# Kernel tuning notes

Measured on AMD Instinct MI355X. Metric: run time of the kernel, lower is better.

Reference implementation:

```python
import jax, jax.numpy as jnp
import numpy as np

B = 4
HIDDEN = 256
NH, NL, NP = 8, 4, 4
DH = HIDDEN // NH
IMG = 256
SHAPES = ((64, 64), (32, 32), (16, 16), (8, 8))
CHS = (128, 256, 512, 512)
T = 3
NLAYERS = 6
S = sum(h * w for h, w in SHAPES)


def conv2d(x, w, b, pad):
    y = jax.lax.conv_general_dilated(x, w, (1, 1), [(pad, pad), (pad, pad)],
                                     dimension_numbers=('NCHW', 'OIHW', 'NCHW'))
    return y + b[None, :, None, None]


def group_norm(x, g, beta, groups=32, eps=1e-5):
    b, c, h, w = x.shape
    xg = x.reshape(b, groups, c // groups, h, w)
    mu = xg.mean((2, 3, 4), keepdims=True)
    var = ((xg - mu) ** 2).mean((2, 3, 4), keepdims=True)
    xg = (xg - mu) * jax.lax.rsqrt(var + eps)
    return xg.reshape(b, c, h, w) * g[None, :, None, None] + beta[None, :, None, None]


def layer_norm(x, g, b, eps=1e-5):
    mu = x.mean(-1, keepdims=True)
    var = ((x - mu) ** 2).mean(-1, keepdims=True)
    return (x - mu) * jax.lax.rsqrt(var + eps) * g + b


def pos_embed_sine(h, w, num_feats=128, temp=10000.0):
    # PositionEmbeddingSine with normalize=True, mask all-False
    scale = 2.0 * np.pi
    eps = 1e-6
    y = jnp.arange(1, h + 1, dtype=jnp.float32) / (h + eps) * scale
    x = jnp.arange(1, w + 1, dtype=jnp.float32) / (w + eps) * scale
    yy = jnp.broadcast_to(y[:, None], (h, w))
    xx = jnp.broadcast_to(x[None, :], (h, w))
    dim_t = temp ** (2.0 * (jnp.arange(num_feats) // 2).astype(jnp.float32) / num_feats)
    px = xx[..., None] / dim_t
    py = yy[..., None] / dim_t
    px = jnp.stack([jnp.sin(px[..., 0::2]), jnp.cos(px[..., 1::2])], -1).reshape(h, w, num_feats)
    py = jnp.stack([jnp.sin(py[..., 0::2]), jnp.cos(py[..., 1::2])], -1).reshape(h, w, num_feats)
    return jnp.concatenate([py, px], -1)  # (h, w, 2*num_feats)


def ms_deform(value, locs, attw):
    # value: (B,S,NH,DH); locs: (B,S,NH,NL,NP,2) normalized xy; attw: (B,S,NH,NL,NP)
    out = jnp.zeros((B, S, NH, DH), value.dtype)
    start = 0
    for l, (h, w) in enumerate(SHAPES):
        v = value[:, start:start + h * w]  # (B,hw,NH,DH)
        start += h * w
        gx = locs[:, :, :, l, :, 0] * w - 0.5  # grid_sample align_corners=False
        gy = locs[:, :, :, l, :, 1] * h - 0.5  # (B,S,NH,NP)
        x0 = jnp.floor(gx)
        y0 = jnp.floor(gy)
        wx1 = gx - x0
        wy1 = gy - y0
        acc = jnp.zeros((B, S, NH, NP, DH), value.dtype)
        for dy in (0, 1):
            for dx in (0, 1):
                xi = x0 + dx
                yi = y0 + dy
                wgt = (wx1 if dx else 1.0 - wx1) * (wy1 if dy else 1.0 - wy1)
                valid = ((xi >= 0) & (xi < w) & (yi >= 0) & (yi < h)).astype(value.dtype)
                xi_c = jnp.clip(xi, 0, w - 1).astype(jnp.int32)
                yi_c = jnp.clip(yi, 0, h - 1).astype(jnp.int32)
                idx = yi_c * w + xi_c  # (B,S,NH,NP)
                idx2 = idx.transpose(0, 1, 3, 2).reshape(B, S * NP, NH, 1)
                samp = jnp.take_along_axis(v, idx2, axis=1)  # (B,S*NP,NH,DH)
                samp = samp.reshape(B, S, NP, NH, DH).transpose(0, 1, 3, 2, 4)
                acc = acc + samp * (wgt * valid)[..., None]
        out = out + (acc * attw[:, :, :, l, :, None]).sum(3)
    return out.reshape(B, S, NH * DH)


def _forward(feat_t0_l0, feat_t0_l1, feat_t0_l2, feat_t0_l3,
             feat_t1_l0, feat_t1_l1, feat_t1_l2, feat_t1_l3,
             feat_t2_l0, feat_t2_l1, feat_t2_l2, feat_t2_l3,
             tfw,
             proj_w0, proj_b0, gn_g0, gn_b0,
             proj_w1, proj_b1, gn_g1, gn_b1,
             proj_w2, proj_b2, gn_g2, gn_b2,
             proj_w3, proj_b3, gn_g3, gn_b3,
             level_embed,
             off_w, off_b, aw_w, aw_b, val_w, val_b, out_w, out_b,
             ln1_g, ln1_b, ff1_w, ff1_b, ff2_w, ff2_b, ln2_g, ln2_b,
             c1_w, c1_b, c2_w, c2_b):
    feats = [[feat_t0_l0, feat_t0_l1, feat_t0_l2, feat_t0_l3],
             [feat_t1_l0, feat_t1_l1, feat_t1_l2, feat_t1_l3],
             [feat_t2_l0, feat_t2_l1, feat_t2_l2, feat_t2_l3]]
    proj = [(proj_w0, proj_b0, gn_g0, gn_b0), (proj_w1, proj_b1, gn_g1, gn_b1),
            (proj_w2, proj_b2, gn_g2, gn_b2), (proj_w3, proj_b3, gn_g3, gn_b3)]
    priors = (0, CHS[0], CHS[1], CHS[2])  # replicates original (buggy) prior indexing
    srcs, poss = [], []
    for l in range(NL):
        atf = jnp.stack([feats[t][l] for t in range(T)], 1)  # (B,T,C,H,W)
        wsl = jax.nn.softmax(tfw[:, priors[l]:priors[l] + CHS[l]], axis=0)  # (T,C)
        fused = (atf * wsl[None, :, :, None, None]).sum(1)
        pw, pb, gg, gb = proj[l]
        x = group_norm(conv2d(fused, pw, pb, 0), gg, gb)  # 1x1 proj + GN
        h, w = SHAPES[l]
        srcs.append(x.reshape(B, HIDDEN, h * w).transpose(0, 2, 1))
        pe = pos_embed_sine(h, w).reshape(h * w, HIDDEN) + level_embed[l]
        poss.append(jnp.broadcast_to(pe[None], (B, h * w, HIDDEN)))
    src = jnp.concatenate(srcs, 1)  # (B,S,256)
    pos = jnp.concatenate(poss, 1)
    # reference points (valid_ratios == 1 since masks are all False)
    refs = []
    for (h, w) in SHAPES:
        gy, gx = jnp.meshgrid((jnp.arange(h) + 0.5) / h, (jnp.arange(w) + 0.5) / w, indexing='ij')
        refs.append(jnp.stack([gx.ravel(), gy.ravel()], -1))
    ref = jnp.broadcast_to(jnp.concatenate(refs, 0)[None, :, None, :], (B, S, NL, 2)).astype(jnp.float32)
    norm_wh = jnp.array([[w, h] for (h, w) in SHAPES], jnp.float32)  # (NL,2) xy
    for i in range(NLAYERS):
        q = src + pos
        off = (q @ off_w[i].T + off_b[i]).reshape(B, S, NH, NL, NP, 2)
        aw = jax.nn.softmax((q @ aw_w[i].T + aw_b[i]).reshape(B, S, NH, NL * NP), -1).reshape(B, S, NH, NL, NP)
        val = (src @ val_w[i].T + val_b[i]).reshape(B, S, NH, DH)
        locs = ref[:, :, None, :, None, :] + off / norm_wh[None, None, None, :, None, :]
        attn = ms_deform(val, locs, aw) @ out_w[i].T + out_b[i]
        src = layer_norm(src + attn, ln1_g[i], ln1_b[i])
        ff = (jax.nn.relu(src @ ff1_w[i].T + ff1_b[i])) @ ff2_w[i].T + ff2_b[i]
        src = layer_norm(src + ff, ln2_g[i], ln2_b[i])
    h0, w0 = SHAPES[0]
    layer0 = src[:, :h0 * w0, :].reshape(B, h0, w0, HIDDEN).transpose(0, 3, 1, 2)
    pred = conv2d(jax.nn.relu(conv2d(layer0, c1_w, c1_b, 1)), c2_w, c2_b, 1)
    return jax.image.resize(pred, (B, pred.shape[1], IMG, IMG), method='bilinear')


def setup_inputs():
    key = jax.random.key(0)
    ks = iter(jax.random.split(key, 128))
    d = {}
    for t in range(T):
        for l, ((h, w), c) in enumerate(zip(SHAPES, CHS)):
            d['feat_t%d_l%d' % (t, l)] = jax.random.normal(next(ks), (B, c, h, w), jnp.float32)
    d['tfw'] = jax.random.normal(next(ks), (T, sum(CHS)), jnp.float32)
    for l, c in enumerate(CHS):
        d['proj_w%d' % l] = jax.random.normal(next(ks), (HIDDEN, c, 1, 1), jnp.float32) * 0.02
        d['proj_b%d' % l] = jnp.zeros((HIDDEN,), jnp.float32)
        d['gn_g%d' % l] = jnp.ones((HIDDEN,), jnp.float32)
        d['gn_b%d' % l] = jnp.zeros((HIDDEN,), jnp.float32)
    d['level_embed'] = jax.random.normal(next(ks), (NL, HIDDEN), jnp.float32)
    Lc = NLAYERS

    def w(shape, s=0.02):
        return jax.random.normal(next(ks), shape, jnp.float32) * s
    d['off_w'] = w((Lc, NH * NL * NP * 2, HIDDEN))
    d['off_b'] = w((Lc, NH * NL * NP * 2), 0.1)
    d['aw_w'] = w((Lc, NH * NL * NP, HIDDEN))
    d['aw_b'] = w((Lc, NH * NL * NP), 0.1)
    d['val_w'] = w((Lc, HIDDEN, HIDDEN))
    d['val_b'] = jnp.zeros((Lc, HIDDEN), jnp.float32)
    d['out_w'] = w((Lc, HIDDEN, HIDDEN))
    d['out_b'] = jnp.zeros((Lc, HIDDEN), jnp.float32)
    d['ln1_g'] = jnp.ones((Lc, HIDDEN), jnp.float32)
    d['ln1_b'] = jnp.zeros((Lc, HIDDEN), jnp.float32)
    d['ff1_w'] = w((Lc, 1024, HIDDEN))
    d['ff1_b'] = jnp.zeros((Lc, 1024), jnp.float32)
    d['ff2_w'] = w((Lc, HIDDEN, 1024))
    d['ff2_b'] = jnp.zeros((Lc, HIDDEN), jnp.float32)
    d['ln2_g'] = jnp.ones((Lc, HIDDEN), jnp.float32)
    d['ln2_b'] = jnp.zeros((Lc, HIDDEN), jnp.float32)
    d['c1_w'] = w((64, HIDDEN, 3, 3))
    d['c1_b'] = jnp.zeros((64,), jnp.float32)
    d['c2_w'] = w((2, 64, 3, 3))
    d['c2_b'] = jnp.zeros((2,), jnp.float32)
    return d


def reference(feat_t0_l0, feat_t0_l1, feat_t0_l2, feat_t0_l3,
              feat_t1_l0, feat_t1_l1, feat_t1_l2, feat_t1_l3,
              feat_t2_l0, feat_t2_l1, feat_t2_l2, feat_t2_l3,
              tfw,
              proj_w0, proj_b0, gn_g0, gn_b0,
              proj_w1, proj_b1, gn_g1, gn_b1,
              proj_w2, proj_b2, gn_g2, gn_b2,
              proj_w3, proj_b3, gn_g3, gn_b3,
              level_embed,
              off_w, off_b, aw_w, aw_b, val_w, val_b, out_w, out_b,
              ln1_g, ln1_b, ff1_w, ff1_b, ff2_w, ff2_b, ln2_g, ln2_b,
              c1_w, c1_b, c2_w, c2_b):
    return _forward(feat_t0_l0, feat_t0_l1, feat_t0_l2, feat_t0_l3,
                    feat_t1_l0, feat_t1_l1, feat_t1_l2, feat_t1_l3,
                    feat_t2_l0, feat_t2_l1, feat_t2_l2, feat_t2_l3,
                    tfw,
                    proj_w0, proj_b0, gn_g0, gn_b0,
                    proj_w1, proj_b1, gn_g1, gn_b1,
                    proj_w2, proj_b2, gn_g2, gn_b2,
                    proj_w3, proj_b3, gn_g3, gn_b3,
                    level_embed,
                    off_w, off_b, aw_w, aw_b, val_w, val_b, out_w, out_b,
                    ln1_g, ln1_b, ff1_w, ff1_b, ff2_w, ff2_b, ln2_g, ln2_b,
                    c1_w, c1_b, c2_w, c2_b)
```

## Files before the change

### kernel.cpp

```cpp
#include <hip/hip_runtime.h>
#include <math.h>

constexpr int kB = 4;
constexpr int kS = 5440;
constexpr int kH = 256;
constexpr int kNH = 8, kNL = 4, kNP = 4, kDH = 32;
constexpr int kM = kB * kS;
constexpr int kCHSUM = 1408;

typedef __attribute__((ext_vector_type(8))) short short8v;
typedef __attribute__((ext_vector_type(4))) short short4v;
typedef __attribute__((ext_vector_type(4))) float f32x4;

__device__ inline short bf16rne(float f) {
    unsigned u = __float_as_uint(f);
    u += 0x7FFF + ((u >> 16) & 1);
    return (short)(u >> 16);
}
__device__ inline float bf2f(short s) {
    return __uint_as_float(((unsigned)(unsigned short)s) << 16);
}


__global__ void f2bf_kernel(const float* __restrict__ in, short* __restrict__ out, int n)
{
    int idx = (blockIdx.x * blockDim.x + threadIdx.x) * 4;
    if (idx >= n) return;
    f32x4 v = *(const f32x4*)(in + idx);
    short4v o;
    o[0]=bf16rne(v[0]); o[1]=bf16rne(v[1]); o[2]=bf16rne(v[2]); o[3]=bf16rne(v[3]);
    *(short4v*)(out + idx) = o;
}

__global__ void concat_w_kernel(const float* __restrict__ off_w, const float* __restrict__ aw_w,
                                short* __restrict__ Wcat, int n)
{
    int idx = blockIdx.x * blockDim.x + threadIdx.x;
    if (idx >= n) return;
    int col = idx & 255;
    int row = (idx >> 8) % 384;
    int i   = idx / (384*256);
    float v = (row < 256) ? off_w[((size_t)i*256 + row)*256 + col]
                          : aw_w[((size_t)i*128 + row-256)*256 + col];
    Wcat[idx] = bf16rne(v);
}
__global__ void concat_b_kernel(const float* __restrict__ off_b, const float* __restrict__ aw_b,
                                float* __restrict__ bcat, int n)
{
    int idx = blockIdx.x * blockDim.x + threadIdx.x;
    if (idx >= n) return;
    int row = idx % 384;
    int i   = idx / 384;
    bcat[idx] = (row < 256) ? off_b[i*256 + row] : aw_b[i*128 + row-256];
}

__global__ void reorder_c1w_kernel(const float* __restrict__ w, short* __restrict__ out, int n)
{
    int idx = blockIdx.x * blockDim.x + threadIdx.x;
    if (idx >= n) return;
    int k = idx % 2304, o = idx / 2304;
    int kblk = k >> 8, c = k & 255;
    out[idx] = bf16rne(w[(size_t)o*2304 + c*9 + kblk]);
}
__global__ void reorder_c2w_kernel(const float* __restrict__ w, float* __restrict__ out)
{
    int idx = blockIdx.x * blockDim.x + threadIdx.x;
    if (idx >= 1152) return;
    int c = idx & 63, r = idx >> 6;
    int o = r / 9, kblk = r % 9;
    out[idx] = w[((size_t)o*64 + c)*9 + kblk];
}


__global__ __launch_bounds__(256) void fuseT_kernel(const float* __restrict__ f0,
        const float* __restrict__ f1, const float* __restrict__ f2,
        const float* __restrict__ tfw, short* __restrict__ out,
        int c, int hw, int prior)
{
    __shared__ float tile[32][33];
    int p0 = blockIdx.x * 32;
    int c0 = blockIdx.y * 32;
    int b  = blockIdx.z;
    int tx  = threadIdx.x & 31;
    int ty8 = threadIdx.x >> 5;
    #pragma unroll
    for (int i = 0; i < 4; ++i) {
        int ch = c0 + ty8 + i*8;
        float t0 = tfw[0*kCHSUM + prior + ch];
        float t1 = tfw[1*kCHSUM + prior + ch];
        float t2 = tfw[2*kCHSUM + prior + ch];
        float m = fmaxf(t0, fmaxf(t1, t2));
        float e0 = expf(t0-m), e1 = expf(t1-m), e2 = expf(t2-m);
        float inv = 1.0f / (e0+e1+e2);
        size_t base = ((size_t)b*c + ch)*hw + p0 + tx;
        tile[ty8+i*8][tx] = f0[base]*(e0*inv) + f1[base]*(e1*inv) + f2[base]*(e2*inv);
    }
    __syncthreads();
    #pragma unroll
    for (int i = 0; i < 4; ++i) {
        int p = p0 + ty8 + i*8;
        out[((size_t)b*hw + p)*c + c0 + tx] = bf16rne(tile[tx][ty8+i*8]);
    }
}

__global__ __launch_bounds__(256) void gn_sum_kernel(const float* __restrict__ xbufT,
        float* __restrict__ gnstat, int nchunks)
{
    int chunk = blockIdx.x, b = blockIdx.y;
    int t = threadIdx.x;
    size_t base = ((size_t)b*nchunks + chunk) * 4096;
    float s = 0.f, q = 0.f;
    #pragma unroll
    for (int i = 0; i < 4; ++i) {
        f32x4 v = *(const f32x4*)(xbufT + base + i*1024 + t*4);
        s += v[0]+v[1]+v[2]+v[3];
        q += v[0]*v[0]+v[1]*v[1]+v[2]*v[2]+v[3]*v[3];
    }
    __shared__ float ls[256], lq[256];
    ls[t] = s; lq[t] = q; __syncthreads();
    if (t < 64) { ls[t] += ls[t+64]+ls[t+128]+ls[t+192];
                  lq[t] += lq[t+64]+lq[t+128]+lq[t+192]; }
    __syncthreads();
    if (t < 32) {
        float ss = ls[2*t] + ls[2*t+1];
        float qq = lq[2*t] + lq[2*t+1];
        size_t o = (((size_t)b*nchunks + chunk)*32 + t)*2;
        gnstat[o] = ss; gnstat[o+1] = qq;
    }
}

__global__ __launch_bounds__(256) void gn_fin_kernel(const float* __restrict__ gnstat,
        const float* __restrict__ gg, const float* __restrict__ gb,
        float* __restrict__ gnA, float* __restrict__ gnB, int nchunks, int hw)
{
    int b = blockIdx.x, t = threadIdx.x;
    int g = t >> 3, sub = t & 7;
    float s = 0.f, q = 0.f;
    for (int c = sub; c < nchunks; c += 8) {
        size_t o = (((size_t)b*nchunks + c)*32 + g)*2;
        s += gnstat[o]; q += gnstat[o+1];
    }
    __shared__ float ls[256], lq[256], gmu[32], ginv[32];
    ls[t] = s; lq[t] = q; __syncthreads();
    if (sub < 4) { ls[t] += ls[t+4]; lq[t] += lq[t+4]; } __syncthreads();
    if (sub < 2) { ls[t] += ls[t+2]; lq[t] += lq[t+2]; } __syncthreads();
    if (sub == 0) {
        float ss = ls[t] + ls[t+1], qq = lq[t] + lq[t+1];
        float n = 8.0f * hw;
        float mu = ss / n;
        float var = qq / n - mu*mu;
        gmu[g] = mu; ginv[g] = rsqrtf(var + 1e-5f);
    }
    __syncthreads();
    int ch = t;
    float A = ginv[ch>>3] * gg[ch];
    float B = gb[ch] - gmu[ch>>3] * A;
    gnA[b*256 + ch] = A;
    gnB[b*256 + ch] = B;
}

__global__ __launch_bounds__(256) void gn_apply_kernel(const float* __restrict__ xbufT,
        const float* __restrict__ gnA, const float* __restrict__ gnB,
        const float* __restrict__ pos, float* __restrict__ src,
        short* __restrict__ srcbf, short* __restrict__ qbf, int hw, int sbase)
{
    int E = hw * 256;
    size_t fl = (size_t)blockIdx.x*1024 + threadIdx.x*4;
    int b = (int)(fl / E);
    int off = (int)(fl - (size_t)b*E);
    int p = off >> 8, col = off & 255;
    f32x4 v = *(const f32x4*)(xbufT + fl);
    f32x4 A = *(const f32x4*)(gnA + b*256 + col);
    f32x4 Bv = *(const f32x4*)(gnB + b*256 + col);
    size_t si = ((size_t)b*kS + sbase + p)*256 + col;
    f32x4 pv = *(const f32x4*)(pos + si);
    f32x4 o;
    o[0]=v[0]*A[0]+Bv[0]; o[1]=v[1]*A[1]+Bv[1];
    o[2]=v[2]*A[2]+Bv[2]; o[3]=v[3]*A[3]+Bv[3];
    *(f32x4*)(src + si) = o;
    short4v sb, qb;
    sb[0]=bf16rne(o[0]); sb[1]=bf16rne(o[1]); sb[2]=bf16rne(o[2]); sb[3]=bf16rne(o[3]);
    qb[0]=bf16rne(o[0]+pv[0]); qb[1]=bf16rne(o[1]+pv[1]);
    qb[2]=bf16rne(o[2]+pv[2]); qb[3]=bf16rne(o[3]+pv[3]);
    *(short4v*)(srcbf + si) = sb;
    *(short4v*)(qbf + si) = qb;
}

__global__ void pos_kernel(const float* __restrict__ lev, float* __restrict__ pos,
                           int h, int w, int sbase, int lvl, int n)
{
    int idx = blockIdx.x * blockDim.x + threadIdx.x;
    if (idx >= n) return;
    int ch = idx % kH;
    int p  = idx / kH;
    int py = p / w, px = p % w;
    int c2 = ch & 127;
    int i  = c2 >> 1;
    float invdt = exp2f((float)i * -0.20762050593046015f);
    float t;
    if (ch < 128) t = (py + 1) / ((float)h + 1e-6f) * 6.2831853071795864f;
    else          t = (px + 1) / ((float)w + 1e-6f) * 6.2831853071795864f;
    float arg = t * invdt;
    float val = (c2 & 1) ? cosf(arg) : sinf(arg);
    val += lev[lvl*kH + ch];
    for (int b = 0; b < kB; ++b)
        pos[((size_t)b*kS + sbase + p)*kH + ch] = val;
}

template<int BN, int OUTMODE>
__global__ __launch_bounds__(256) void gemm_big(const short* __restrict__ A,
        const short* __restrict__ W, const float* __restrict__ bias,
        float* __restrict__ C, short* __restrict__ Cb, int N, int K, int relu)
{
    constexpr int FJ = BN / 32;
    constexpr int NBV = (BN == 128) ? 4 : 2;
    __shared__ short Asm[2][128 * 40];
    __shared__ short Bsm[2][BN * 40];
    const int t    = threadIdx.x;
    const int bn   = blockIdx.x * BN;
    const int bm   = blockIdx.y * 128;
    const int lane = t & 63;
    const int wid  = t >> 6;
    const int wr   = wid >> 1;
    const int wc   = wid & 1;
    const int frow = lane & 15;
    const int g    = lane >> 4;
    const int sa_r = t >> 1;
    const int sa_p = t & 1;

    f32x4 acc[4][FJ];
    #pragma unroll
    for (int i = 0; i < 4; ++i)
        #pragma unroll
        for (int j = 0; j < FJ; ++j)
            acc[i][j] = (f32x4){0.f,0.f,0.f,0.f};

    const short* Aptr = A + (size_t)(bm + sa_r)*K + sa_p*32;
    short8v a[4], b[NBV];
    #pragma unroll
    for (int v = 0; v < 4; ++v) a[v] = *(const short8v*)(Aptr + v*8);

    int sb_r, sb_p, sb_o;
    const short* Wptr;
    if constexpr (BN == 128) {
        sb_r = t >> 1; sb_p = t & 1; sb_o = 0;
        Wptr = W + (size_t)(bn + sb_r)*K + sb_p*32;
    } else {
        sb_r = t >> 2; sb_p = (t & 3) >> 1; sb_o = (t & 1) * 16;
        Wptr = W + (size_t)(bn + sb_r)*K + (t & 3)*16;
    }
    #pragma unroll
    for (int v = 0; v < NBV; ++v) b[v] = *(const short8v*)(Wptr + v*8);

    for (int k0 = 0; k0 < K; k0 += 64) {
        __syncthreads();
        #pragma unroll
        for (int v = 0; v < 4; ++v) *(short8v*)&Asm[sa_p][sa_r*40 + v*8] = a[v];
        #pragma unroll
        for (int v = 0; v < NBV; ++v) *(short8v*)&Bsm[sb_p][sb_r*40 + sb_o + v*8] = b[v];
        __syncthreads();
        if (k0 + 64 < K) {
            #pragma unroll
            for (int v = 0; v < 4; ++v) a[v] = *(const short8v*)(Aptr + k0 + 64 + v*8);
            #pragma unroll
            for (int v = 0; v < NBV; ++v) b[v] = *(const short8v*)(Wptr + k0 + 64 + v*8);
        }
        #pragma unroll
        for (int p = 0; p < 2; ++p) {
            short8v af[4], bfv[FJ];
            #pragma unroll
            for (int i = 0; i < 4; ++i)
                af[i] = *(const short8v*)&Asm[p][(wr*64 + i*16 + frow)*40 + g*8];
            #pragma unroll
            for (int j = 0; j < FJ; ++j)
                bfv[j] = *(const short8v*)&Bsm[p][(wc*(BN/2) + j*16 + frow)*40 + g*8];
            #pragma unroll
            for (int i = 0; i < 4; ++i)
                #pragma unroll
                for (int j = 0; j < FJ; ++j)
                    acc[i][j] = __builtin_amdgcn_mfma_f32_16x16x32_bf16(af[i], bfv[j], acc[i][j], 0, 0, 0);
        }
    }

    #pragma unroll
    for (int j = 0; j < FJ; ++j) {
        int col = bn + wc*(BN/2) + j*16 + frow;
        float bz = bias[col];
        #pragma unroll
        for (int i = 0; i < 4; ++i) {
            int row = bm + wr*64 + i*16 + g*4;
            #pragma unroll
            for (int rr = 0; rr < 4; ++rr) {
                float v = acc[i][j][rr] + bz;
                if (relu) v = fmaxf(v, 0.f);
                if constexpr (OUTMODE == 0) C[(size_t)(row + rr)*N + col] = v;
                else                        Cb[(size_t)(row + rr)*N + col] = bf16rne(v);
            }
        }
    }
}

__global__ __launch_bounds__(256) void gemm_qv(const short* __restrict__ Aq,
        const short* __restrict__ As, const short* __restrict__ W1,
        const short* __restrict__ W2, const float* __restrict__ b1,
        const float* __restrict__ b2, float* __restrict__ C1,
        short* __restrict__ Cb2)
{
    __shared__ short Asm[2][128 * 40];
    __shared__ short Bsm[2][128 * 40];
    const int t    = threadIdx.x;
    const int bn   = blockIdx.x * 128;
    const int bm   = blockIdx.y * 128;
    const bool qreg = bn < 384;
    const int K = 256;
    const int lane = t & 63;
    const int wid  = t >> 6;
    const int wr   = wid >> 1;
    const int wc   = wid & 1;
    const int frow = lane & 15;
    const int g    = lane >> 4;
    const int sa_r = t >> 1;
    const int sa_p = t & 1;

    f32x4 acc[4][4];
    #pragma unroll
    for (int i = 0; i < 4; ++i)
        #pragma unroll
        for (int j = 0; j < 4; ++j)
            acc[i][j] = (f32x4){0.f,0.f,0.f,0.f};

    const short* Aptr = (qreg ? Aq : As) + (size_t)(bm + sa_r)*K + sa_p*32;
    const short* Wptr = (qreg ? (W1 + (size_t)(bn + sa_r)*K)
                              : (W2 + (size_t)(bn - 384 + sa_r)*K)) + sa_p*32;
    short8v a[4], b[4];
    #pragma unroll
    for (int v = 0; v < 4; ++v) { a[v] = *(const short8v*)(Aptr + v*8);
                                  b[v] = *(const short8v*)(Wptr + v*8); }

    for (int k0 = 0; k0 < K; k0 += 64) {
        __syncthreads();
        #pragma unroll
        for (int v = 0; v < 4; ++v) {
            *(short8v*)&Asm[sa_p][sa_r*40 + v*8] = a[v];
            *(short8v*)&Bsm[sa_p][sa_r*40 + v*8] = b[v];
        }
        __syncthreads();
        if (k0 + 64 < K) {
            #pragma unroll
            for (int v = 0; v < 4; ++v) {
                a[v] = *(const short8v*)(Aptr + k0 + 64 + v*8);
                b[v] = *(const short8v*)(Wptr + k0 + 64 + v*8);
            }
        }
        #pragma unroll
        for (int p = 0; p < 2; ++p) {
            short8v af[4], bfv[4];
            #pragma unroll
            for (int i = 0; i < 4; ++i)
                af[i] = *(const short8v*)&Asm[p][(wr*64 + i*16 + frow)*40 + g*8];
            #pragma unroll
            for (int j = 0; j < 4; ++j)
                bfv[j] = *(const short8v*)&Bsm[p][(wc*64 + j*16 + frow)*40 + g*8];
            #pragma unroll
            for (int i = 0; i < 4; ++i)
                #pragma unroll
                for (int j = 0; j < 4; ++j)
                    acc[i][j] = __builtin_amdgcn_mfma_f32_16x16x32_bf16(af[i], bfv[j], acc[i][j], 0, 0, 0);
        }
    }

    if (bn == 256) {
        #pragma unroll
        for (int j = 0; j < 4; ++j) {
            int col = bn + wc*64 + j*16 + frow;
            float bz = b1[col];
            #pragma unroll
            for (int i = 0; i < 4; ++i) {
                int row = bm + wr*64 + i*16 + g*4;
                #pragma unroll
                for (int rr = 0; rr < 4; ++rr) {
                    float v = acc[i][j][rr] + bz;
                    float m = v;
                    m = fmaxf(m, __shfl_xor(m, 1));
                    m = fmaxf(m, __shfl_xor(m, 2));
                    m = fmaxf(m, __shfl_xor(m, 4));
                    m = fmaxf(m, __shfl_xor(m, 8));
                    float e = expf(v - m);
                    float s = e;
                    s += __shfl_xor(s, 1);
                    s += __shfl_xor(s, 2);
                    s += __shfl_xor(s, 4);
                    s += __shfl_xor(s, 8);
                    C1[(size_t)(row + rr)*384 + col] = e / s;
                }
            }
        }
    } else {
        #pragma unroll
        for (int j = 0; j < 4; ++j) {
            int col = bn + wc*64 + j*16 + frow;
            float bz = qreg ? b1[col] : b2[col - 384];
            #pragma unroll
            for (int i = 0; i < 4; ++i) {
                int row = bm + wr*64 + i*16 + g*4;
                #pragma unroll
                for (int rr = 0; rr < 4; ++rr) {
                    float v = acc[i][j][rr] + bz;
                    if (qreg) C1[(size_t)(row + rr)*384 + col] = v;
                    else      Cb2[(size_t)(row + rr)*256 + col - 384] = bf16rne(v);
                }
            }
        }
    }
}

__global__ __launch_bounds__(256) void conv1_gemm_kernel(const short* __restrict__ srcbf,
        const short* __restrict__ Wr, const float* __restrict__ bias,
        float* __restrict__ C)
{
    __shared__ short Asm[2][128 * 40];
    __shared__ short Bsm[2][64 * 40];
    const int t    = threadIdx.x;
    const int bm   = blockIdx.x * 128;
    const int K    = 2304;
    const int lane = t & 63;
    const int wid  = t >> 6;
    const int wr   = wid >> 1;
    const int wc   = wid & 1;
    const int frow = lane & 15;
    const int g    = lane >> 4;
    const int sa_r = t >> 1;
    const int sa_p = t & 1;

    const int m  = bm + sa_r;
    const int bb = m >> 12, ys = (m >> 6) & 63, xs = m & 63;

    f32x4 acc[4][2];
    #pragma unroll
    for (int i = 0; i < 4; ++i)
        #pragma unroll
        for (int j = 0; j < 2; ++j)
            acc[i][j] = (f32x4){0.f,0.f,0.f,0.f};

    auto loadA = [&](int k0, short8v* r) {
        int kk = k0 + sa_p*32;
        int kblk = kk >> 8;
        int dyy = kblk / 3, dxx = kblk - dyy*3;
        int yy = ys + dyy - 1, xx = xs + dxx - 1;
        if (yy >= 0 && yy < 64 && xx >= 0 && xx < 64) {
            const short* p = srcbf + ((size_t)(bb*kS + yy*64 + xx))*256 + (kk & 255);
            #pragma unroll
            for (int v = 0; v < 4; ++v) r[v] = *(const short8v*)(p + v*8);
        } else {
            #pragma unroll
            for (int v = 0; v < 4; ++v) r[v] = (short8v){0,0,0,0,0,0,0,0};
        }
    };

    const int sb_r = t >> 2, sb_p = (t & 3) >> 1, sb_o = (t & 1) * 16;
    const short* Wptr = Wr + (size_t)sb_r*K + (t & 3)*16;
    short8v a[4], b[2];
    loadA(0, a);
    b[0] = *(const short8v*)Wptr;
    b[1] = *(const short8v*)(Wptr + 8);

    for (int k0 = 0; k0 < K; k0 += 64) {
        __syncthreads();
        #pragma unroll
        for (int v = 0; v < 4; ++v) *(short8v*)&Asm[sa_p][sa_r*40 + v*8] = a[v];
        *(short8v*)&Bsm[sb_p][sb_r*40 + sb_o]     = b[0];
        *(short8v*)&Bsm[sb_p][sb_r*40 + sb_o + 8] = b[1];
        __syncthreads();
        if (k0 + 64 < K) {
            loadA(k0 + 64, a);
            b[0] = *(const short8v*)(Wptr + k0 + 64);
            b[1] = *(const short8v*)(Wptr + k0 + 72);
        }
        #pragma unroll
        for (int p = 0; p < 2; ++p) {
            short8v af[4], bfv[2];
            #pragma unroll
            for (int i = 0; i < 4; ++i)
                af[i] = *(const short8v*)&Asm[p][(wr*64 + i*16 + frow)*40 + g*8];
            #pragma unroll
            for (int j = 0; j < 2; ++j)
                bfv[j] = *(const short8v*)&Bsm[p][(wc*32 + j*16 + frow)*40 + g*8];
            #pragma unroll
            for (int i = 0; i < 4; ++i)
                #pragma unroll
                for (int j = 0; j < 2; ++j)
                    acc[i][j] = __builtin_amdgcn_mfma_f32_16x16x32_bf16(af[i], bfv[j], acc[i][j], 0, 0, 0);
        }
    }

    #pragma unroll
    for (int j = 0; j < 2; ++j) {
        int col = wc*32 + j*16 + frow;
        float bz = bias[col];
        #pragma unroll
        for (int i = 0; i < 4; ++i) {
            int row = bm + wr*64 + i*16 + g*4;
            #pragma unroll
            for (int rr = 0; rr < 4; ++rr) {
                float v = fmaxf(acc[i][j][rr] + bz, 0.f);
                C[(size_t)(row + rr)*64 + col] = v;
            }
        }
    }
}

__global__ __launch_bounds__(256) void msdeform8_kernel(const short* __restrict__ val,
        const float* __restrict__ cat, short* __restrict__ msd)
{
    int tid  = threadIdx.x;
    int d8   = tid & 3;
    int head = (tid >> 2) & 7;
    int bs   = blockIdx.x*8 + (tid >> 5);
    int s  = bs % kS;
    int b  = bs / kS;
    float refx, refy;
    if (s < 4096)      { int loc = s;        refy = ((loc>>6)+0.5f)/64.f; refx = ((loc&63)+0.5f)/64.f; }
    else if (s < 5120) { int loc = s - 4096; refy = ((loc>>5)+0.5f)/32.f; refx = ((loc&31)+0.5f)/32.f; }
    else if (s < 5376) { int loc = s - 5120; refy = ((loc>>4)+0.5f)/16.f; refx = ((loc&15)+0.5f)/16.f; }
    else               { int loc = s - 5376; refy = ((loc>>3)+0.5f)/8.f;  refx = ((loc&7)+0.5f)/8.f; }
    const float* op = cat + (size_t)bs*384 + head*32;
    const float* ap = cat + (size_t)bs*384 + 256 + head*16;
    const short* vb = val + (size_t)b*kS*256 + head*32 + d8*8;
    const int WL[4] = {64,32,16,8};
    const int BASE[4] = {0,4096,5120,5376};
    float acc[8] = {0.f,0.f,0.f,0.f,0.f,0.f,0.f,0.f};
    #pragma unroll
    for (int l = 0; l < 4; ++l) {
        int wl = WL[l], base = BASE[l];
        f32x4 o0 = *(const f32x4*)(op + l*8);
        f32x4 o1 = *(const f32x4*)(op + l*8 + 4);
        f32x4 av = *(const f32x4*)(ap + l*4);
        float oxs[4] = {o0[0], o0[2], o1[0], o1[2]};
        float oys[4] = {o0[1], o0[3], o1[1], o1[3]};
        #pragma unroll
        for (int p = 0; p < 4; ++p) {
            float gx = (refx + oxs[p]/wl)*wl - 0.5f;
            float gy = (refy + oys[p]/wl)*wl - 0.5f;
            float x0f = floorf(gx), y0f = floorf(gy);
            float wx1 = gx - x0f, wy1 = gy - y0f;
            int x0 = (int)x0f, y0 = (int)y0f;
            float a = av[p];
            #pragma unroll
            for (int dy = 0; dy < 2; ++dy) {
                int yi = y0 + dy;
                float wy = dy ? wy1 : 1.f - wy1;
                int vyok = (yi >= 0) & (yi < wl);
                int yc = min(max(yi, 0), wl - 1);
                #pragma unroll
                for (int dx = 0; dx < 2; ++dx) {
                    int xi = x0 + dx;
                    float wx = dx ? wx1 : 1.f - wx1;
                    int vok = vyok & (xi >= 0) & (xi < wl);
                    int xc = min(max(xi, 0), wl - 1);
                    float wgt = vok ? wx*wy*a : 0.f;
                    uint4 v = *(const uint4*)&vb[(size_t)(base + yc*wl + xc)*256];
                    acc[0] = fmaf(__uint_as_float(v.x << 16),          wgt, acc[0]);
                    acc[1] = fmaf(__uint_as_float(v.x & 0xffff0000u), wgt, acc[1]);
                    acc[2] = fmaf(__uint_as_float(v.y << 16),          wgt, acc[2]);
                    acc[3] = fmaf(__uint_as_float(v.y & 0xffff0000u), wgt, acc[3]);
                    acc[4] = fmaf(__uint_as_float(v.z << 16),          wgt, acc[4]);
                    acc[5] = fmaf(__uint_as_float(v.z & 0xffff0000u), wgt, acc[5]);
                    acc[6] = fmaf(__uint_as_float(v.w << 16),          wgt, acc[6]);
                    acc[7] = fmaf(__uint_as_float(v.w & 0xffff0000u), wgt, acc[7]);
                }
            }
        }
    }
    short8v o;
    #pragma unroll
    for (int k = 0; k < 8; ++k) o[k] = bf16rne(acc[k]);
    *(short8v*)&msd[(size_t)bs*256 + head*32 + d8*8] = o;
}

template<int WQ>
__global__ __launch_bounds__(256) void add_ln_kernel(float* __restrict__ src,
        const short* __restrict__ delta, const float* __restrict__ g,
        const float* __restrict__ bta, short* __restrict__ srcbf,
        short* __restrict__ qbf, const float* __restrict__ pos)
{
    int lane = threadIdx.x & 63;
    int row  = blockIdx.x*4 + (threadIdx.x >> 6);
    f32x4* s4 = (f32x4*)(src + (size_t)row*256);
    f32x4 x = s4[lane];
    short4v dd = *(const short4v*)&delta[(size_t)row*256 + lane*4];
    x[0]+=bf2f(dd[0]); x[1]+=bf2f(dd[1]); x[2]+=bf2f(dd[2]); x[3]+=bf2f(dd[3]);
    float s = x[0]+x[1]+x[2]+x[3];
    #pragma unroll
    for (int o = 1; o < 64; o <<= 1) s += __shfl_xor(s, o);
    float mu = s * (1.f/256.f);
    f32x4 xc;
    xc[0]=x[0]-mu; xc[1]=x[1]-mu; xc[2]=x[2]-mu; xc[3]=x[3]-mu;
    float s2 = xc[0]*xc[0]+xc[1]*xc[1]+xc[2]*xc[2]+xc[3]*xc[3];
    #pragma unroll
    for (int o = 1; o < 64; o <<= 1) s2 += __shfl_xor(s2, o);
    float inv = rsqrtf(s2*(1.f/256.f) + 1e-5f);
    const f32x4 gv = ((const f32x4*)g)[lane];
    const f32x4 bv = ((const f32x4*)bta)[lane];
    f32x4 o4;
    o4[0]=xc[0]*inv*gv[0]+bv[0]; o4[1]=xc[1]*inv*gv[1]+bv[1];
    o4[2]=xc[2]*inv*gv[2]+bv[2]; o4[3]=xc[3]*inv*gv[3]+bv[3];
    s4[lane] = o4;
    short4v sb;
    sb[0]=bf16rne(o4[0]); sb[1]=bf16rne(o4[1]); sb[2]=bf16rne(o4[2]); sb[3]=bf16rne(o4[3]);
    *(short4v*)&srcbf[(size_t)row*256 + lane*4] = sb;
    if constexpr (WQ) {
        f32x4 pv = ((const f32x4*)(pos + (size_t)row*256))[lane];
        short4v qb;
        qb[0]=bf16rne(o4[0]+pv[0]); qb[1]=bf16rne(o4[1]+pv[1]);
        qb[2]=bf16rne(o4[2]+pv[2]); qb[3]=bf16rne(o4[3]+pv[3]);
        *(short4v*)&qbf[(size_t)row*256 + lane*4] = qb;
    }
}

__global__ void conv2_kernel(const float* __restrict__ c1, const float* __restrict__ w,
                             const float* __restrict__ bias, float* __restrict__ pred)
{
    int idx = blockIdx.x * blockDim.x + threadIdx.x;
    int x = idx & 63;
    int y = (idx >> 6) & 63;
    int o = (idx >> 12) & 1;
    int b = idx >> 13;
    float acc = bias[o];
    #pragma unroll
    for (int dy = 0; dy < 3; ++dy) {
        int yy = y + dy - 1;
        if (yy < 0 || yy >= 64) continue;
        #pragma unroll
        for (int dx = 0; dx < 3; ++dx) {
            int xx = x + dx - 1;
            if (xx < 0 || xx >= 64) continue;
            const f32x4* sp = (const f32x4*)(c1 + ((size_t)(b*4096) + yy*64 + xx)*64);
            const f32x4* wp = (const f32x4*)(w + (o*9 + dy*3 + dx)*64);
            #pragma unroll
            for (int c = 0; c < 16; ++c) {
                f32x4 sv = sp[c], wv = wp[c];
                acc += sv[0]*wv[0] + sv[1]*wv[1] + sv[2]*wv[2] + sv[3]*wv[3];
            }
        }
    }
    pred[idx] = acc;
}

__global__ void resize_kernel(const float* __restrict__ pred, float* __restrict__ out)
{
    int idx = blockIdx.x * blockDim.x + threadIdx.x;
    int X = idx & 255;
    int Y = (idx >> 8) & 255;
    int c = (idx >> 16) & 1;
    int b = idx >> 17;
    float sx = (X + 0.5f)*0.25f - 0.5f;
    float sy = (Y + 0.5f)*0.25f - 0.5f;
    int x0 = (int)floorf(sx); float fx = sx - x0;
    int y0 = (int)floorf(sy); float fy = sy - y0;
    int x0c = min(max(x0, 0), 63), x1c = min(max(x0+1, 0), 63);
    int y0c = min(max(y0, 0), 63), y1c = min(max(y0+1, 0), 63);
    const float* p = pred + ((size_t)(b*2 + c))*4096;
    float v00 = p[y0c*64 + x0c], v01 = p[y0c*64 + x1c];
    float v10 = p[y1c*64 + x0c], v11 = p[y1c*64 + x1c];
    out[idx] = (1.f-fy)*((1.f-fx)*v00 + fx*v01) + fy*((1.f-fx)*v10 + fx*v11);
}

extern "C" void kernel_launch(void* const* d_in, const int* in_sizes, int n_in,
                              void* d_out, int out_size, void* d_ws, size_t ws_size,
                              hipStream_t stream)
{
    const float* F[3][4];
    for (int t = 0; t < 3; ++t)
        for (int l = 0; l < 4; ++l)
            F[t][l] = (const float*)d_in[t*4 + l];
    const float* tfw = (const float*)d_in[12];
    const float *pw[4], *pb[4], *gg[4], *gb[4];
    for (int l = 0; l < 4; ++l) {
        pw[l] = (const float*)d_in[13 + 4*l];
        pb[l] = (const float*)d_in[14 + 4*l];
        gg[l] = (const float*)d_in[15 + 4*l];
        gb[l] = (const float*)d_in[16 + 4*l];
    }
    const float* lev   = (const float*)d_in[29];
    const float* off_w = (const float*)d_in[30];
    const float* off_b = (const float*)d_in[31];
    const float* aw_w  = (const float*)d_in[32];
    const float* aw_b  = (const float*)d_in[33];
    const float* val_w = (const float*)d_in[34];
    const float* val_b = (const float*)d_in[35];
    const float* out_w = (const float*)d_in[36];
    const float* out_b = (const float*)d_in[37];
    const float* ln1g  = (const float*)d_in[38];
    const float* ln1b  = (const float*)d_in[39];
    const float* ff1w  = (const float*)d_in[40];
    const float* ff1b  = (const float*)d_in[41];
    const float* ff2w  = (const float*)d_in[42];
    const float* ff2b  = (const float*)d_in[43];
    const float* ln2g  = (const float*)d_in[44];
    const float* ln2b  = (const float*)d_in[45];
    const float* c1w   = (const float*)d_in[46];
    const float* c1b   = (const float*)d_in[47];
    const float* c2w   = (const float*)d_in[48];
    const float* c2b   = (const float*)d_in[49];

    const size_t N256 = (size_t)kB * kS * 256;
    float* ws    = (float*)d_ws;
    float* src   = ws;
    short* srcbf = (short*)(src + N256);
    short* qbf   = srcbf + N256;
    short* valbf = qbf + N256;
    short* msdbf = valbf + N256;
    short* warena= msdbf + N256;
    short* Wcat_bf = warena;
    short* valw_bf = Wcat_bf + 589824;
    short* outw_bf = valw_bf + 393216;
    short* ff1w_bf = outw_bf + 393216;
    short* ff2w_bf = ff1w_bf + 1572864;
    short* pw_bf   = ff2w_bf + 1572864;
    short* c1w_bf  = pw_bf + 360448;
    float* bcat  = (float*)(c1w_bf + 147456 + 128);
    float* gnstat= bcat + 4096;
    float* gnA   = gnstat + 65536;
    float* gnB   = gnA + 1024;
    float* c2wr  = gnB + 1024;
    float* pos   = c2wr + 1280;
    float* cat   = pos + N256;
    float* tmp   = cat + (size_t)kM*384;
    short* tmpbf = (short*)tmp;
    short* ffhbf = (short*)(tmp + N256);
    short* fusedT = (short*)cat;
    float* xbufT  = tmp;
    float* c1o   = (float*)valbf;
    float* pred  = (float*)msdbf;

    const int LVL_HWS[4]  = {4096, 1024, 256, 64};
    const int LVL_BASE[4] = {0, 4096, 5120, 5376};
    const int LVL_C[4]    = {128, 256, 512, 512};
    const int LVL_PRIOR[4]= {0, 128, 256, 512};
    const int PW_OFF[4]   = {0, 32768, 98304, 229376};

    {
        int n = 6*384*256;
        concat_w_kernel<<<(n+255)/256, 256, 0, stream>>>(off_w, aw_w, Wcat_bf, n);
        concat_b_kernel<<<(6*384+255)/256, 256, 0, stream>>>(off_b, aw_b, bcat, 6*384);
        f2bf_kernel<<<(393216/4+255)/256, 256, 0, stream>>>(val_w, valw_bf, 393216);
        f2bf_kernel<<<(393216/4+255)/256, 256, 0, stream>>>(out_w, outw_bf, 393216);
        f2bf_kernel<<<(1572864/4+255)/256, 256, 0, stream>>>(ff1w, ff1w_bf, 1572864);
        f2bf_kernel<<<(1572864/4+255)/256, 256, 0, stream>>>(ff2w, ff2w_bf, 1572864);
        for (int l = 0; l < 4; ++l) {
            int n2 = 256 * LVL_C[l];
            f2bf_kernel<<<(n2/4+255)/256, 256, 0, stream>>>(pw[l], pw_bf + PW_OFF[l], n2);
        }
        reorder_c1w_kernel<<<(147456+255)/256, 256, 0, stream>>>(c1w, c1w_bf, 147456);
        reorder_c2w_kernel<<<(1152+255)/256, 256, 0, stream>>>(c2w, c2wr);
    }

    for (int l = 0; l < 4; ++l) {
        int hw = LVL_HWS[l];
        int dim = (l==0)?64:(l==1)?32:(l==2)?16:8;
        int n3 = hw * kH;
        pos_kernel<<<(n3+255)/256, 256, 0, stream>>>(lev, pos, dim, dim, LVL_BASE[l], l, n3);
    }
    for (int l = 0; l < 4; ++l) {
        int hw = LVL_HWS[l], c = LVL_C[l];
        dim3 gf(hw/32, c/32, kB);
        fuseT_kernel<<<gf, 256, 0, stream>>>(F[0][l], F[1][l], F[2][l], tfw,
                                             fusedT, c, hw, LVL_PRIOR[l]);
        dim3 gp(4, (kB*hw)/128);
        gemm_big<64,0><<<gp, 256, 0, stream>>>(fusedT, pw_bf + PW_OFF[l], pb[l],
                                               xbufT, nullptr, 256, c, 0);
        int nchunks = hw / 16;
        gn_sum_kernel<<<dim3(nchunks, kB), 256, 0, stream>>>(xbufT, gnstat, nchunks);
        gn_fin_kernel<<<kB, 256, 0, stream>>>(gnstat, gg[l], gb[l], gnA, gnB, nchunks, hw);
        gn_apply_kernel<<<(kB*hw*256)/1024, 256, 0, stream>>>(xbufT, gnA, gnB, pos,
                                                              src, srcbf, qbf, hw, LVL_BASE[l]);
    }

    for (int i = 0; i < 6; ++i) {
        gemm_qv<<<dim3(5, kM/128), 256, 0, stream>>>(qbf, srcbf,
                Wcat_bf + (size_t)i*384*256, valw_bf + (size_t)i*65536,
                bcat + i*384, val_b + i*256, cat, valbf);
        msdeform8_kernel<<<kM/8, 256, 0, stream>>>(valbf, cat, msdbf);
        gemm_big<64,1><<<dim3(4, kM/128), 256, 0, stream>>>(msdbf, outw_bf + (size_t)i*65536,
                                                      out_b + i*256, nullptr, tmpbf, 256, 256, 0);
        add_ln_kernel<0><<<kM/4, 256, 0, stream>>>(src, tmpbf, ln1g + i*256, ln1b + i*256,
                                                   srcbf, nullptr, nullptr);
        gemm_big<128,1><<<dim3(8, kM/128), 256, 0, stream>>>(srcbf, ff1w_bf + (size_t)i*262144,
                                                       ff1b + i*1024, nullptr, ffhbf, 1024, 256, 1);
        gemm_big<64,1><<<dim3(4, kM/128), 256, 0, stream>>>(ffhbf, ff2w_bf + (size_t)i*262144,
                                                      ff2b + i*256, nullptr, tmpbf, 256, 1024, 0);
        add_ln_kernel<1><<<kM/4, 256, 0, stream>>>(src, tmpbf, ln2g + i*256, ln2b + i*256,
                                                   srcbf, qbf, pos);
    }

    {
        conv1_gemm_kernel<<<128, 256, 0, stream>>>(srcbf, c1w_bf, c1b, c1o);
        conv2_kernel<<<(kB*2*64*64)/256, 256, 0, stream>>>(c1o, c2wr, c2b, pred);
        resize_kernel<<<(kB*2*256*256)/256, 256, 0, stream>>>(pred, (float*)d_out);
    }
}
```

Before: 1.196 ms.

## Switch GEMMs to 32x32 MFMA with swizzled LDS and XCD-aware block mapping

Rewrites the GEMM kernels to use 32x32x16 bf16 MFMA tiles instead of 16x16x32. The output tile changes from 128xBN to BMx128, so N=256 GEMMs now use a 64x128 tile. LDS addresses get an XOR swizzle to reduce bank conflicts, and a 1D grid with XCD-aware remapping is added to the GEMMs and msdeform for better L2 locality across chiplets. The changes aim at MFMA issue efficiency and memory locality, but the new epilogue writes rows with a strided pattern and register pressure may rise.

```diff
diff --git a/kernel.cpp b/kernel.cpp
--- a/kernel.cpp
+++ b/kernel.cpp
@@ -11,6 +11,7 @@
 typedef __attribute__((ext_vector_type(8))) short short8v;
 typedef __attribute__((ext_vector_type(4))) short short4v;
 typedef __attribute__((ext_vector_type(4))) float f32x4;
+typedef __attribute__((ext_vector_type(16))) float f32x16;
 
 __device__ inline short bf16rne(float f) {
     unsigned u = __float_as_uint(f);
@@ -20,6 +21,12 @@
 __device__ inline float bf2f(short s) {
     return __uint_as_float(((unsigned)(unsigned short)s) << 16);
 }
+__device__ inline int xcd_swz(int orig, int nwg) {
+    int q = nwg >> 3, r = nwg & 7;
+    int x = orig & 7, o = orig >> 3;
+    return (x < r ? x*(q+1) : r*(q+1) + (x-r)*q) + o;
+}
+#define LSWZ(row, chunk) ((row)*40 + ((chunk) ^ ((row) & 24)))
 
 
 __global__ void f2bf_kernel(const float* __restrict__ in, short* __restrict__ out, int n)
@@ -207,100 +214,106 @@
         pos[((size_t)b*kS + sbase + p)*kH + ch] = val;
 }
 
-template<int BN, int OUTMODE>
-__global__ __launch_bounds__(256) void gemm_big(const short* __restrict__ A,
+template<int BM, int OUTMODE>
+__global__ __launch_bounds__(256) void gemm32(const short* __restrict__ A,
         const short* __restrict__ W, const float* __restrict__ bias,
-        float* __restrict__ C, short* __restrict__ Cb, int N, int K, int relu)
-{
-    constexpr int FJ = BN / 32;
-    constexpr int NBV = (BN == 128) ? 4 : 2;
-    __shared__ short Asm[2][128 * 40];
-    __shared__ short Bsm[2][BN * 40];
+        float* __restrict__ C, short* __restrict__ Cb, int N, int K, int relu, int ncols)
+{
+    constexpr int FI = BM / 64;
+    constexpr int NAV = (BM == 128) ? 4 : 2;
+    __shared__ short Asm[2][BM * 40];
+    __shared__ short Bsm[2][128 * 40];
+    const int lin = xcd_swz(blockIdx.x, gridDim.x);
+    const int bn  = (lin % ncols) * 128;
+    const int bm  = (lin / ncols) * BM;
     const int t    = threadIdx.x;
-    const int bn   = blockIdx.x * BN;
-    const int bm   = blockIdx.y * 128;
     const int lane = t & 63;
     const int wid  = t >> 6;
     const int wr   = wid >> 1;
     const int wc   = wid & 1;
-    const int frow = lane & 15;
-    const int g    = lane >> 4;
-    const int sa_r = t >> 1;
-    const int sa_p = t & 1;
-
-    f32x4 acc[4][FJ];
-    #pragma unroll
-    for (int i = 0; i < 4; ++i)
-        #pragma unroll
-        for (int j = 0; j < FJ; ++j)
-            acc[i][j] = (f32x4){0.f,0.f,0.f,0.f};
-
-    const short* Aptr = A + (size_t)(bm + sa_r)*K + sa_p*32;
-    short8v a[4], b[NBV];
-    #pragma unroll
-    for (int v = 0; v < 4; ++v) a[v] = *(const short8v*)(Aptr + v*8);
-
-    int sb_r, sb_p, sb_o;
-    const short* Wptr;
-    if constexpr (BN == 128) {
-        sb_r = t >> 1; sb_p = t & 1; sb_o = 0;
-        Wptr = W + (size_t)(bn + sb_r)*K + sb_p*32;
-    } else {
-        sb_r = t >> 2; sb_p = (t & 3) >> 1; sb_o = (t & 1) * 16;
-        Wptr = W + (size_t)(bn + sb_r)*K + (t & 3)*16;
-    }
-    #pragma unroll
-    for (int v = 0; v < NBV; ++v) b[v] = *(const short8v*)(Wptr + v*8);
+    const int l31  = lane & 31;
+    const int hi8  = (lane >> 5) * 8;
+
+    f32x16 acc[FI][2];
+    #pragma unroll
+    for (int i = 0; i < FI; ++i)
+        #pragma unroll
+        for (int j = 0; j < 2; ++j)
+            acc[i][j] = (f32x16){0,0,0,0,0,0,0,0,0,0,0,0,0,0,0,0};
+
+    int sa_r, sa_k;
+    if constexpr (BM == 128) { sa_r = t >> 1; sa_k = (t & 1) * 32; }
+    else                     { sa_r = t >> 2; sa_k = (t & 3) * 16; }
+    const short* Aptr = A + (size_t)(bm + sa_r)*K + sa_k;
+    const int sb_r = t >> 1;
+    const int sb_k = (t & 1) * 32;
+    const short* Wptr = W + (size_t)(bn + sb_r)*K + sb_k;
+
+    short8v a[NAV], b[4];
+    #pragma unroll
+    for (int v = 0; v < NAV; ++v) a[v] = *(const short8v*)(Aptr + v*8);
+    #pragma unroll
+    for (int v = 0; v < 4; ++v)   b[v] = *(const short8v*)(Wptr + v*8);
 
     for (int k0 = 0; k0 < K; k0 += 64) {
         __syncthreads();
-        #pragma unroll
-        for (int v = 0; v < 4; ++v) *(short8v*)&Asm[sa_p][sa_r*40 + v*8] = a[v];
-        #pragma unroll
-        for (int v = 0; v < NBV; ++v) *(short8v*)&Bsm[sb_p][sb_r*40 + sb_o + v*8] = b[v];
+        if constexpr (BM == 128) {
+            #pragma unroll
+            for (int v = 0; v < 4; ++v) *(short8v*)&Asm[t & 1][LSWZ(sa_r, v*8)] = a[v];
+        } else {
+            #pragma unroll
+            for (int v = 0; v < 2; ++v)
+                *(short8v*)&Asm[sa_k >> 5][LSWZ(sa_r, (sa_k & 16) + v*8)] = a[v];
+        }
+        #pragma unroll
+        for (int v = 0; v < 4; ++v) *(short8v*)&Bsm[t & 1][LSWZ(sb_r, v*8)] = b[v];
         __syncthreads();
         if (k0 + 64 < K) {
             #pragma unroll
-            for (int v = 0; v < 4; ++v) a[v] = *(const short8v*)(Aptr + k0 + 64 + v*8);
-            #pragma unroll
-            for (int v = 0; v < NBV; ++v) b[v] = *(const short8v*)(Wptr + k0 + 64 + v*8);
-        }
-        #pragma unroll
-        for (int p = 0; p < 2; ++p) {
-            short8v af[4], bfv[FJ];
-            #pragma unroll
-            for (int i = 0; i < 4; ++i)
-                af[i] = *(const short8v*)&Asm[p][(wr*64 + i*16 + frow)*40 + g*8];
-            #pragma unroll
-            for (int j = 0; j < FJ; ++j)
-                bfv[j] = *(const short8v*)&Bsm[p][(wc*(BN/2) + j*16 + frow)*40 + g*8];
-            #pragma unroll
-            for (int i = 0; i < 4; ++i)
-                #pragma unroll
-                for (int j = 0; j < FJ; ++j)
-                    acc[i][j] = __builtin_amdgcn_mfma_f32_16x16x32_bf16(af[i], bfv[j], acc[i][j], 0, 0, 0);
-        }
-    }
-
-    #pragma unroll
-    for (int j = 0; j < FJ; ++j) {
-        int col = bn + wc*(BN/2) + j*16 + frow;
+            for (int v = 0; v < NAV; ++v) a[v] = *(const short8v*)(Aptr + k0 + 64 + v*8);
+            #pragma unroll
+            for (int v = 0; v < 4; ++v)   b[v] = *(const short8v*)(Wptr + k0 + 64 + v*8);
+        }
+        #pragma unroll
+        for (int p = 0; p < 2; ++p)
+            #pragma unroll
+            for (int ks = 0; ks < 2; ++ks) {
+                short8v af[FI], bfv[2];
+                #pragma unroll
+                for (int i = 0; i < FI; ++i)
+                    af[i] = *(const short8v*)&Asm[p][LSWZ(wr*(BM/2) + i*32 + l31, ks*16 + hi8)];
+                #pragma unroll
+                for (int j = 0; j < 2; ++j)
+                    bfv[j] = *(const short8v*)&Bsm[p][LSWZ(wc*64 + j*32 + l31, ks*16 + hi8)];
+                #pragma unroll
+                for (int i = 0; i < FI; ++i)
+                    #pragma unroll
+                    for (int j = 0; j < 2; ++j)
+                        acc[i][j] = __builtin_amdgcn_mfma_f32_32x32x16_bf16(af[i], bfv[j], acc[i][j], 0, 0, 0);
+            }
+    }
+
+    const int rbase = 4 * (lane >> 5);
+    #pragma unroll
+    for (int j = 0; j < 2; ++j) {
+        int col = bn + wc*64 + j*32 + l31;
         float bz = bias[col];
         #pragma unroll
-        for (int i = 0; i < 4; ++i) {
-            int row = bm + wr*64 + i*16 + g*4;
-            #pragma unroll
-            for (int rr = 0; rr < 4; ++rr) {
-                float v = acc[i][j][rr] + bz;
+        for (int i = 0; i < FI; ++i) {
+            int row0 = bm + wr*(BM/2) + i*32 + rbase;
+            #pragma unroll
+            for (int r = 0; r < 16; ++r) {
+                int row = row0 + (r & 3) + 8*(r >> 2);
+                float v = acc[i][j][r] + bz;
                 if (relu) v = fmaxf(v, 0.f);
-                if constexpr (OUTMODE == 0) C[(size_t)(row + rr)*N + col] = v;
-                else                        Cb[(size_t)(row + rr)*N + col] = bf16rne(v);
+                if constexpr (OUTMODE == 0) C[(size_t)row*N + col] = v;
+                else                        Cb[(size_t)row*N + col] = bf16rne(v);
             }
         }
     }
 }
 
-__global__ __launch_bounds__(256) void gemm_qv(const short* __restrict__ Aq,
+__global__ __launch_bounds__(256) void gemm_qv32(const short* __restrict__ Aq,
         const short* __restrict__ As, const short* __restrict__ W1,
         const short* __restrict__ W2, const float* __restrict__ b1,
         const float* __restrict__ b2, float* __restrict__ C1,
@@ -308,26 +321,27 @@
 {
     __shared__ short Asm[2][128 * 40];
     __shared__ short Bsm[2][128 * 40];
-    const int t    = threadIdx.x;
-    const int bn   = blockIdx.x * 128;
-    const int bm   = blockIdx.y * 128;
+    const int lin = xcd_swz(blockIdx.x, gridDim.x);
+    const int bn  = (lin % 5) * 128;
+    const int bm  = (lin / 5) * 128;
     const bool qreg = bn < 384;
     const int K = 256;
+    const int t    = threadIdx.x;
     const int lane = t & 63;
     const int wid  = t >> 6;
     const int wr   = wid >> 1;
     const int wc   = wid & 1;
-    const int frow = lane & 15;
-    const int g    = lane >> 4;
+    const int l31  = lane & 31;
+    const int hi8  = (lane >> 5) * 8;
     const int sa_r = t >> 1;
     const int sa_p = t & 1;
 
-    f32x4 acc[4][4];
-    #pragma unroll
-    for (int i = 0; i < 4; ++i)
-        #pragma unroll
-        for (int j = 0; j < 4; ++j)
-            acc[i][j] = (f32x4){0.f,0.f,0.f,0.f};
+    f32x16 acc[2][2];
+    #pragma unroll
+    for (int i = 0; i < 2; ++i)
+        #pragma unroll
+        for (int j = 0; j < 2; ++j)
+            acc[i][j] = (f32x16){0,0,0,0,0,0,0,0,0,0,0,0,0,0,0,0};
 
     const short* Aptr = (qreg ? Aq : As) + (size_t)(bm + sa_r)*K + sa_p*32;
     const short* Wptr = (qreg ? (W1 + (size_t)(bn + sa_r)*K)
@@ -341,8 +355,8 @@
         __syncthreads();
         #pragma unroll
         for (int v = 0; v < 4; ++v) {
-            *(short8v*)&Asm[sa_p][sa_r*40 + v*8] = a[v];
-            *(short8v*)&Bsm[sa_p][sa_r*40 + v*8] = b[v];
+            *(short8v*)&Asm[sa_p][LSWZ(sa_r, v*8)] = a[v];
+            *(short8v*)&Bsm[sa_p][LSWZ(sa_r, v*8)] = b[v];
         }
         __syncthreads();
         if (k0 + 64 < K) {
@@ -353,33 +367,37 @@
             }
         }
         #pragma unroll
-        for (int p = 0; p < 2; ++p) {
-            short8v af[4], bfv[4];
-            #pragma unroll
-            for (int i = 0; i < 4; ++i)
-                af[i] = *(const short8v*)&Asm[p][(wr*64 + i*16 + frow)*40 + g*8];
-            #pragma unroll
-            for (int j = 0; j < 4; ++j)
-                bfv[j] = *(const short8v*)&Bsm[p][(wc*64 + j*16 + frow)*40 + g*8];
-            #pragma unroll
-            for (int i = 0; i < 4; ++i)
-                #pragma unroll
-                for (int j = 0; j < 4; ++j)
-                    acc[i][j] = __builtin_amdgcn_mfma_f32_16x16x32_bf16(af[i], bfv[j], acc[i][j], 0, 0, 0);
-        }
-    }
-
+        for (int p = 0; p < 2; ++p)
+            #pragma unroll
+            for (int ks = 0; ks < 2; ++ks) {
+                short8v af[2], bfv[2];
+                #pragma unroll
+                for (int i = 0; i < 2; ++i)
+                    af[i] = *(const short8v*)&Asm[p][LSWZ(wr*64 + i*32 + l31, ks*16 + hi8)];
+                #pragma unroll
+                for (int j = 0; j < 2; ++j)
+                    bfv[j] = *(const short8v*)&Bsm[p][LSWZ(wc*64 + j*32 + l31, ks*16 + hi8)];
+                #pragma unroll
+                for (int i = 0; i < 2; ++i)
+                    #pragma unroll
+                    for (int j = 0; j < 2; ++j)
+                        acc[i][j] = __builtin_amdgcn_mfma_f32_32x32x16_bf16(af[i], bfv[j], acc[i][j], 0, 0, 0);
+            }
+    }
+
+    const int rbase = 4 * (lane >> 5);
     if (bn == 256) {
         #pragma unroll
-        for (int j = 0; j < 4; ++j) {
-            int col = bn + wc*64 + j*16 + frow;
+        for (int j = 0; j < 2; ++j) {
+            int col = bn + wc*64 + j*32 + l31;
             float bz = b1[col];
             #pragma unroll
-            for (int i = 0; i < 4; ++i) {
-                int row = bm + wr*64 + i*16 + g*4;
-                #pragma unroll
-                for (int rr = 0; rr < 4; ++rr) {
-                    float v = acc[i][j][rr] + bz;
+            for (int i = 0; i < 2; ++i) {
+                int row0 = bm + wr*64 + i*32 + rbase;
+                #pragma unroll
+                for (int r = 0; r < 16; ++r) {
+                    int row = row0 + (r & 3) + 8*(r >> 2);
+                    float v = acc[i][j][r] + bz;
                     float m = v;
                     m = fmaxf(m, __shfl_xor(m, 1));
                     m = fmaxf(m, __shfl_xor(m, 2));
@@ -391,23 +409,24 @@
                     s += __shfl_xor(s, 2);
                     s += __shfl_xor(s, 4);
                     s += __shfl_xor(s, 8);
-                    C1[(size_t)(row + rr)*384 + col] = e / s;
+                    C1[(size_t)row*384 + col] = e / s;
                 }
             }
         }
     } else {
         #pragma unroll
-        for (int j = 0; j < 4; ++j) {
-            int col = bn + wc*64 + j*16 + frow;
+        for (int j = 0; j < 2; ++j) {
+            int col = bn + wc*64 + j*32 + l31;
             float bz = qreg ? b1[col] : b2[col - 384];
             #pragma unroll
-            for (int i = 0; i < 4; ++i) {
-                int row = bm + wr*64 + i*16 + g*4;
-                #pragma unroll
-                for (int rr = 0; rr < 4; ++rr) {
-                    float v = acc[i][j][rr] + bz;
-                    if (qreg) C1[(size_t)(row + rr)*384 + col] = v;
-                    else      Cb2[(size_t)(row + rr)*256 + col - 384] = bf16rne(v);
+            for (int i = 0; i < 2; ++i) {
+                int row0 = bm + wr*64 + i*32 + rbase;
+                #pragma unroll
+                for (int r = 0; r < 16; ++r) {
+                    int row = row0 + (r & 3) + 8*(r >> 2);
+                    float v = acc[i][j][r] + bz;
+                    if (qreg) C1[(size_t)row*384 + col] = v;
+                    else      Cb2[(size_t)row*256 + col - 384] = bf16rne(v);
                 }
             }
         }
@@ -512,10 +531,11 @@
 __global__ __launch_bounds__(256) void msdeform8_kernel(const short* __restrict__ val,
         const float* __restrict__ cat, short* __restrict__ msd)
 {
+    int blk  = xcd_swz(blockIdx.x, gridDim.x);
     int tid  = threadIdx.x;
     int d8   = tid & 3;
     int head = (tid >> 2) & 7;
-    int bs   = blockIdx.x*8 + (tid >> 5);
+    int bs   = blk*8 + (tid >> 5);
     int s  = bs % kS;
     int b  = bs / kS;
     float refx, refy;
@@ -766,9 +786,9 @@
         dim3 gf(hw/32, c/32, kB);
         fuseT_kernel<<<gf, 256, 0, stream>>>(F[0][l], F[1][l], F[2][l], tfw,
                                              fusedT, c, hw, LVL_PRIOR[l]);
-        dim3 gp(4, (kB*hw)/128);
-        gemm_big<64,0><<<gp, 256, 0, stream>>>(fusedT, pw_bf + PW_OFF[l], pb[l],
-                                               xbufT, nullptr, 256, c, 0);
+        int nwg = 2 * (kB*hw/64);
+        gemm32<64,0><<<nwg, 256, 0, stream>>>(fusedT, pw_bf + PW_OFF[l], pb[l],
+                                              xbufT, nullptr, 256, c, 0, 2);
         int nchunks = hw / 16;
         gn_sum_kernel<<<dim3(nchunks, kB), 256, 0, stream>>>(xbufT, gnstat, nchunks);
         gn_fin_kernel<<<kB, 256, 0, stream>>>(gnstat, gg[l], gb[l], gnA, gnB, nchunks, hw);
@@ -777,18 +797,18 @@
     }
 
     for (int i = 0; i < 6; ++i) {
-        gemm_qv<<<dim3(5, kM/128), 256, 0, stream>>>(qbf, srcbf,
+        gemm_qv32<<<5*(kM/128), 256, 0, stream>>>(qbf, srcbf,
                 Wcat_bf + (size_t)i*384*256, valw_bf + (size_t)i*65536,
                 bcat + i*384, val_b + i*256, cat, valbf);
         msdeform8_kernel<<<kM/8, 256, 0, stream>>>(valbf, cat, msdbf);
-        gemm_big<64,1><<<dim3(4, kM/128), 256, 0, stream>>>(msdbf, outw_bf + (size_t)i*65536,
-                                                      out_b + i*256, nullptr, tmpbf, 256, 256, 0);
+        gemm32<64,1><<<2*(kM/64), 256, 0, stream>>>(msdbf, outw_bf + (size_t)i*65536,
+                                                    out_b + i*256, nullptr, tmpbf, 256, 256, 0, 2);
         add_ln_kernel<0><<<kM/4, 256, 0, stream>>>(src, tmpbf, ln1g + i*256, ln1b + i*256,
                                                    srcbf, nullptr, nullptr);
-        gemm_big<128,1><<<dim3(8, kM/128), 256, 0, stream>>>(srcbf, ff1w_bf + (size_t)i*262144,
-                                                       ff1b + i*1024, nullptr, ffhbf, 1024, 256, 1);
-        gemm_big<64,1><<<dim3(4, kM/128), 256, 0, stream>>>(ffhbf, ff2w_bf + (size_t)i*262144,
-                                                      ff2b + i*256, nullptr, tmpbf, 256, 1024, 0);
+        gemm32<128,1><<<8*(kM/128), 256, 0, stream>>>(srcbf, ff1w_bf + (size_t)i*262144,
+                                                      ff1b + i*1024, nullptr, ffhbf, 1024, 256, 1, 8);
+        gemm32<64,1><<<2*(kM/64), 256, 0, stream>>>(ffhbf, ff2w_bf + (size_t)i*262144,
+                                                    ff2b + i*256, nullptr, tmpbf, 256, 1024, 0, 2);
         add_ln_kernel<1><<<kM/4, 256, 0, stream>>>(src, tmpbf, ln2g + i*256, ln2b + i*256,
                                                    srcbf, qbf, pos);
     }
```

Result: faster. 1.132 ms (-5.4%).
